# Optimization experiments

Measured on AMD Instinct MI355X. Metric: run time of the kernel, lower is better.

## Reference

```python
import jax, jax.numpy as jnp
import numpy as np

E = 6        # num_experts
C = 256      # embed_dim (expert in_channels)
HID = 256    # mlp_dim (expert hidden_channels)
META = 9
GATE_H = 128
BN_EPS = 1e-5  # torch BatchNorm2d default


def _conv(x, w):
    # x: [1,Cin,H,W], w: [Cout,Cin,3,3] -> [1,Cout,H,W], padding=1
    return jax.lax.conv_general_dilated(
        x, w, window_strides=(1, 1), padding=((1, 1), (1, 1)),
        dimension_numbers=("NCHW", "OIHW", "NCHW"))


def _bn(x, mean, var, gamma, beta):
    # inference-mode BatchNorm2d over channel dim
    scale = gamma * jax.lax.rsqrt(var + BN_EPS)
    return (x - mean[None, :, None, None]) * scale[None, :, None, None] + beta[None, :, None, None]


def setup_inputs() -> dict:
    key = jax.random.key(0)
    ks = jax.random.split(key, 20)
    B, H, W = 16, 64, 64
    f32 = jnp.float32
    return {
        "moe_c4": jax.random.normal(ks[0], (B, C, H, W), f32),
        "meta": jax.random.normal(ks[1], (B, META), f32),
        # Gate MLP: Linear(9,128) -> ReLU -> Linear(128,6)
        "gate_w1": jax.random.normal(ks[2], (META, GATE_H), f32) * 0.3,
        "gate_b1": jnp.zeros((GATE_H,), f32),
        "gate_w2": jax.random.normal(ks[3], (GATE_H, E), f32) * 0.1,
        "gate_b2": jnp.zeros((E,), f32),
        # Expert conv1: Conv2d(C, HID, 3) + BN(HID), stacked over experts
        "conv1_w": jax.random.normal(ks[4], (E, HID, C, 3, 3), f32) * 0.02,
        "conv1_b": jnp.zeros((E, HID), f32),
        "bn1_g": jnp.ones((E, HID), f32) + 0.1 * jax.random.normal(ks[5], (E, HID), f32),
        "bn1_b": 0.1 * jax.random.normal(ks[6], (E, HID), f32),
        "bn1_m": 0.1 * jax.random.normal(ks[7], (E, HID), f32),
        "bn1_v": jax.random.uniform(ks[8], (E, HID), f32) + 0.5,
        # Expert conv2: Conv2d(HID, C, 3) + BN(C)
        "conv2_w": jax.random.normal(ks[9], (E, C, HID, 3, 3), f32) * 0.02,
        "conv2_b": jnp.zeros((E, C), f32),
        "bn2_g": jnp.ones((E, C), f32) + 0.1 * jax.random.normal(ks[10], (E, C), f32),
        "bn2_b": 0.1 * jax.random.normal(ks[11], (E, C), f32),
        "bn2_m": 0.1 * jax.random.normal(ks[12], (E, C), f32),
        "bn2_v": jax.random.uniform(ks[13], (E, C), f32) + 0.5,
    }


def reference(moe_c4, meta, gate_w1, gate_b1, gate_w2, gate_b2,
              conv1_w, conv1_b, bn1_g, bn1_b, bn1_m, bn1_v,
              conv2_w, conv2_b, bn2_g, bn2_b, bn2_m, bn2_v):
    # --- Gate: MLP -> softmax -> top-1 routing ---
    h = jax.nn.relu(meta @ gate_w1 + gate_b1)
    gate_probs = jax.nn.softmax(h @ gate_w2 + gate_b2, axis=-1)  # [B,E]
    top1 = jnp.argmax(gate_probs, axis=-1)                        # [B]

    # --- Dispatch: gather each sample's expert params, run one conv stack per sample ---
    def one(x, w1, b1, g1, be1, m1, v1, w2, b2, g2, be2, m2, v2):
        y = _conv(x[None], w1) + b1[None, :, None, None]
        y = jax.nn.relu(_bn(y, m1, v1, g1, be1))
        y = _conv(y, w2) + b2[None, :, None, None]
        y = jax.nn.relu(_bn(y, m2, v2, g2, be2))
        return y[0]

    out = jax.vmap(one)(
        moe_c4,
        conv1_w[top1], conv1_b[top1], bn1_g[top1], bn1_b[top1], bn1_m[top1], bn1_v[top1],
        conv2_w[top1], conv2_b[top1], bn2_g[top1], bn2_b[top1], bn2_m[top1], bn2_v[top1])

    # --- Load-balance loss (torch.std is unbiased -> ddof=1) ---
    importance = gate_probs.sum(axis=0) / (gate_probs.sum() + 1e-8)
    balance_loss = jnp.std(importance, ddof=1)
    return out, balance_loss
```

## Files before the change

kernel.cpp:

```cpp
#include <hip/hip_runtime.h>
#include <hip/hip_bf16.h>

typedef unsigned short u16;
typedef unsigned int u32;
typedef __attribute__((ext_vector_type(8))) short short8_v;
typedef __attribute__((ext_vector_type(4))) float float4_v;

__device__ __forceinline__ u16 f2bf(float f) {
  u32 u = __float_as_uint(f);
  return (u16)((u + 0x7fffu + ((u >> 16) & 1u)) >> 16);
}

__device__ __forceinline__ void gl_lds16(const void* g, void* l) {
  __builtin_amdgcn_global_load_lds(
      (const __attribute__((address_space(1))) u32*)g,
      (__attribute__((address_space(3))) u32*)l, 16, 0, 0);
}

__global__ void gate_kernel(const float* __restrict__ meta,
                            const float* __restrict__ gw1, const float* __restrict__ gb1,
                            const float* __restrict__ gw2, const float* __restrict__ gb2,
                            int* __restrict__ top1, float* __restrict__ loss_out) {
  const int tid = threadIdx.x;
  __shared__ float logits[16][6];
  __shared__ float red[2][6];
  __shared__ float probs[16][6];
  float w2c[6];
  #pragma unroll
  for (int k = 0; k < 6; ++k) w2c[k] = gw2[tid * 6 + k];
  const float b1v = gb1[tid];
  for (int b = 0; b < 16; ++b) {
    float h = b1v;
    #pragma unroll
    for (int i = 0; i < 9; ++i) h += meta[b * 9 + i] * gw1[i * 128 + tid];
    h = fmaxf(h, 0.f);
    float v[6];
    #pragma unroll
    for (int k = 0; k < 6; ++k) v[k] = h * w2c[k];
    #pragma unroll
    for (int off = 32; off >= 1; off >>= 1)
      #pragma unroll
      for (int k = 0; k < 6; ++k) v[k] += __shfl_down(v[k], off, 64);
    if ((tid & 63) == 0)
      for (int k = 0; k < 6; ++k) red[tid >> 6][k] = v[k];
    __syncthreads();
    if (tid < 6) logits[b][tid] = red[0][tid] + red[1][tid] + gb2[tid];
    __syncthreads();
  }
  if (tid < 16) {
    const int b = tid;
    float m = logits[b][0];
    for (int k = 1; k < 6; ++k) m = fmaxf(m, logits[b][k]);
    float s = 0.f, p[6];
    for (int k = 0; k < 6; ++k) { p[k] = expf(logits[b][k] - m); s += p[k]; }
    int best = 0; float bm = p[0];
    for (int k = 1; k < 6; ++k) if (p[k] > bm) { bm = p[k]; best = k; }
    top1[b] = best;
    for (int k = 0; k < 6; ++k) probs[b][k] = p[k] / s;
  }
  __syncthreads();
  if (tid == 0) {
    float col[6] = {0, 0, 0, 0, 0, 0}, tot = 0.f;
    for (int b = 0; b < 16; ++b)
      for (int k = 0; k < 6; ++k) col[k] += probs[b][k];
    for (int k = 0; k < 6; ++k) tot += col[k];
    float imp[6], mean = 0.f;
    for (int k = 0; k < 6; ++k) { imp[k] = col[k] / (tot + 1e-8f); mean += imp[k]; }
    mean *= (1.f / 6.f);
    float var = 0.f;
    for (int k = 0; k < 6; ++k) { float d = imp[k] - mean; var += d * d; }
    loss_out[0] = sqrtf(var * 0.2f);
  }
}

__global__ void fold_kernel(const float* c1b, const float* g1, const float* be1, const float* m1, const float* v1,
                            const float* c2b, const float* g2, const float* be2, const float* m2, const float* v2,
                            float* fold1, float* fold2) {
  int t = blockIdx.x * 256 + threadIdx.x;
  if (t >= 3072) return;
  int conv = t / 1536, r = t % 1536;
  if (conv == 0) {
    float scale = g1[r] * rsqrtf(v1[r] + 1e-5f);
    float shift = (c1b[r] - m1[r]) * scale + be1[r];
    fold1[r * 2] = scale; fold1[r * 2 + 1] = shift;
  } else {
    float scale = g2[r] * rsqrtf(v2[r] + 1e-5f);
    float shift = (c2b[r] - m2[r]) * scale + be2[r];
    fold2[r * 2] = scale; fold2[r * 2 + 1] = shift;
  }
}

__global__ void wprep_kernel(const float* __restrict__ w1, const float* __restrict__ w2,
                             u16* __restrict__ w1t, u16* __restrict__ w2t) {
  const int tid = threadIdx.x;
  const int conv = blockIdx.x >= 1536 ? 1 : 0;
  const int r = blockIdx.x - (conv ? 1536 : 0);
  const int e = r >> 8, co = r & 255;
  const float* src = (conv ? w2 : w1) + (size_t)r * 2304;
  u16* wdst = conv ? w2t : w1t;
  __shared__ float buf[2304];
  const float4* s4 = (const float4*)src;
  for (int k = tid; k < 576; k += 256) ((float4*)buf)[k] = s4[k];
  __syncthreads();
  for (int j = tid; j < 288; j += 256) {
    int tap = j >> 5, ci0 = (j & 31) * 8;
    u16 v[8];
    #pragma unroll
    for (int i = 0; i < 8; ++i) v[i] = f2bf(buf[(ci0 + i) * 9 + tap]);
    int4 pk;
    pk.x = (int)((u32)v[0] | ((u32)v[1] << 16));
    pk.y = (int)((u32)v[2] | ((u32)v[3] << 16));
    pk.z = (int)((u32)v[4] | ((u32)v[5] << 16));
    pk.w = (int)((u32)v[6] | ((u32)v[7] << 16));
    *(int4*)(wdst + (((size_t)e * 9 + tap) * 256 + co) * 256 + ci0) = pk;
  }
}

__global__ void transpose_pad_kernel(const float* __restrict__ x, u16* __restrict__ xpt) {
  const int b = blockIdx.x >> 6, r = blockIdx.x & 63;
  const int tid = threadIdx.x;
  __shared__ u16 tile[64 * 258];
  const int cg = tid & 15, ci_g = tid >> 4;
  const float4* xb4 = (const float4*)(x + ((size_t)b * 256) * 4096 + r * 64);
  #pragma unroll
  for (int k = 0; k < 16; ++k) {
    int ci = k * 16 + ci_g;
    float4 v = xb4[(size_t)ci * 1024 + cg];
    tile[(cg * 4 + 0) * 258 + ci] = f2bf(v.x);
    tile[(cg * 4 + 1) * 258 + ci] = f2bf(v.y);
    tile[(cg * 4 + 2) * 258 + ci] = f2bf(v.z);
    tile[(cg * 4 + 3) * 258 + ci] = f2bf(v.w);
  }
  __syncthreads();
  u16* dstb = xpt + ((size_t)b * 4356 + (size_t)(r + 1) * 66 + 1) * 256;
  #pragma unroll
  for (int it = 0; it < 8; ++it) {
    int chunk = it * 256 + tid;
    int cc = chunk >> 5, part = chunk & 31;
    const u32* lp = (const u32*)(tile + cc * 258 + part * 8);
    int4 vv = {(int)lp[0], (int)lp[1], (int)lp[2], (int)lp[3]};
    *(int4*)(dstb + (size_t)cc * 256 + part * 8) = vv;
  }
}

__global__ void border_zero_kernel(u16* xpt, u16* hpt) {
  int t = blockIdx.x * 256 + threadIdx.x;
  const int TOT = 2 * 16 * 260 * 32;
  if (t >= TOT) return;
  int buf = t / (16 * 260 * 32);
  int r = t % (16 * 260 * 32);
  int b = r / (260 * 32);
  int r2 = r % (260 * 32);
  int idx = r2 >> 5, part = r2 & 31;
  int rc;
  if (idx < 66) rc = idx;
  else if (idx < 132) rc = 65 * 66 + (idx - 66);
  else { int rem = idx - 132; rc = (1 + (rem >> 1)) * 66 + (rem & 1) * 65; }
  u16* base = buf ? hpt : xpt;
  int4 z = {0, 0, 0, 0};
  *(int4*)(base + ((size_t)b * 4356 + rc) * 256 + part * 8) = z;
}

template <int MODE>
__global__ __launch_bounds__(256, 2) void conv_mfma_kernel(
    const u16* __restrict__ src, const u16* __restrict__ wt,
    const int* __restrict__ top1, const float* __restrict__ fold,
    float* __restrict__ outF, u16* __restrict__ outH) {
  __shared__ char Ab[16384];
  __shared__ char Bb[17408];
  const int tid = threadIdx.x;
  const int lane = tid & 63;
  const int wid = tid >> 6;
  const int wr = wid >> 1, wc = wid & 1;
  const int orig = blockIdx.x;
  const int swz = (orig & 7) * 64 + (orig >> 3);
  const int ptile = swz & 31, b = swz >> 5;
  const int e = top1[b];

  const char* srcB0 = (const char*)src + ((size_t)b * 4356 + (size_t)ptile * 132) * 512;
  const char* wA0 = (const char*)wt + (size_t)e * 9 * 65536 * 2;

  float4_v acc[8][4];
  #pragma unroll
  for (int m = 0; m < 8; ++m)
    #pragma unroll
    for (int n = 0; n < 4; ++n)
      acc[m][n] = (float4_v){0.f, 0.f, 0.f, 0.f};

  for (int chunk = 0; chunk < 8; ++chunk) {
    #pragma unroll
    for (int tap = 0; tap < 9; ++tap) {
      __syncthreads();
      if (tap == 0) {
        const char* sB = srcB0 + chunk * 64;
        const int u0 = wid * 256;
        #pragma unroll
        for (int i = 0; i < 4; ++i) {
          int u = u0 + i * 64 + lane;
          int du = u >> 2;
          int qs = (u & 3) ^ ((u >> 3) & 3);
          gl_lds16(sB + (size_t)du * 512 + qs * 16, Bb + (size_t)(u0 + i * 64) * 16);
        }
        if (wid == 0) {
          int u = 1024 + lane;
          int du = u >> 2;
          int qs = (u & 3) ^ ((u >> 3) & 3);
          gl_lds16(sB + (size_t)du * 512 + qs * 16, Bb + 1024 * 16);
        }
      }
      {
        const char* sA = wA0 + (size_t)tap * 131072 + chunk * 64;
        const int u0 = wid * 256;
        #pragma unroll
        for (int i = 0; i < 4; ++i) {
          int u = u0 + i * 64 + lane;
          int cl = u >> 2;
          int qs = (u & 3) ^ ((u >> 3) & 3);
          gl_lds16(sA + (size_t)cl * 512 + qs * 16, Ab + (size_t)(u0 + i * 64) * 16);
        }
      }
      __syncthreads();

      const int kh = tap / 3, kw = tap % 3;
      short8_v bv[4];
      #pragma unroll
      for (int n = 0; n < 4; ++n) {
        int pt = wc * 64 + n * 16 + (lane & 15);
        int rc = ((pt >> 6) + kh) * 66 + (pt & 63) + kw;
        int slot = (lane >> 4) ^ ((rc >> 1) & 3);
        bv[n] = *(const short8_v*)(Bb + rc * 64 + slot * 16);
      }
      #pragma unroll
      for (int m = 0; m < 8; ++m) {
        int cl = wr * 128 + m * 16 + (lane & 15);
        int slot = (lane >> 4) ^ ((cl >> 1) & 3);
        short8_v avm = *(const short8_v*)(Ab + cl * 64 + slot * 16);
        #pragma unroll
        for (int n = 0; n < 4; ++n)
          acc[m][n] = __builtin_amdgcn_mfma_f32_16x16x32_bf16(avm, bv[n], acc[m][n], 0, 0, 0);
      }
    }
  }

  const float* fe = fold + (size_t)e * 512;
  #pragma unroll
  for (int m = 0; m < 8; ++m) {
    const int cb = wr * 128 + m * 16 + ((lane >> 4) << 2);
    float sc0 = fe[(cb + 0) * 2], sh0 = fe[(cb + 0) * 2 + 1];
    float sc1 = fe[(cb + 1) * 2], sh1 = fe[(cb + 1) * 2 + 1];
    float sc2 = fe[(cb + 2) * 2], sh2 = fe[(cb + 2) * 2 + 1];
    float sc3 = fe[(cb + 3) * 2], sh3 = fe[(cb + 3) * 2 + 1];
    #pragma unroll
    for (int n = 0; n < 4; ++n) {
      const int pt = ptile * 128 + wc * 64 + n * 16 + (lane & 15);
      float v0 = fmaxf(acc[m][n][0] * sc0 + sh0, 0.f);
      float v1 = fmaxf(acc[m][n][1] * sc1 + sh1, 0.f);
      float v2 = fmaxf(acc[m][n][2] * sc2 + sh2, 0.f);
      float v3 = fmaxf(acc[m][n][3] * sc3 + sh3, 0.f);
      if (MODE == 1) {
        const size_t rc = (size_t)((pt >> 6) + 1) * 66 + (pt & 63) + 1;
        uint2 pk;
        pk.x = (u32)f2bf(v0) | ((u32)f2bf(v1) << 16);
        pk.y = (u32)f2bf(v2) | ((u32)f2bf(v3) << 16);
        *(uint2*)(outH + ((size_t)b * 4356 + rc) * 256 + cb) = pk;
      } else {
        float* ob = outF + (size_t)b * 1048576;
        ob[(size_t)(cb + 0) * 4096 + pt] = v0;
        ob[(size_t)(cb + 1) * 4096 + pt] = v1;
        ob[(size_t)(cb + 2) * 4096 + pt] = v2;
        ob[(size_t)(cb + 3) * 4096 + pt] = v3;
      }
    }
  }
}

extern "C" void kernel_launch(void* const* d_in, const int* in_sizes, int n_in,
                              void* d_out, int out_size, void* d_ws, size_t ws_size,
                              hipStream_t stream) {
  const float* x    = (const float*)d_in[0];
  const float* meta = (const float*)d_in[1];
  const float* gw1  = (const float*)d_in[2];
  const float* gb1  = (const float*)d_in[3];
  const float* gw2  = (const float*)d_in[4];
  const float* gb2  = (const float*)d_in[5];
  const float* c1w  = (const float*)d_in[6];
  const float* c1b  = (const float*)d_in[7];
  const float* bn1g = (const float*)d_in[8];
  const float* bn1b = (const float*)d_in[9];
  const float* bn1m = (const float*)d_in[10];
  const float* bn1v = (const float*)d_in[11];
  const float* c2w  = (const float*)d_in[12];
  const float* c2b  = (const float*)d_in[13];
  const float* bn2g = (const float*)d_in[14];
  const float* bn2b = (const float*)d_in[15];
  const float* bn2m = (const float*)d_in[16];
  const float* bn2v = (const float*)d_in[17];

  char* ws = (char*)d_ws;
  u16* xpt   = (u16*)(ws);
  u16* hpt   = (u16*)(ws + 35684352);
  u16* w1t   = (u16*)(ws + 71368704);
  u16* w2t   = (u16*)(ws + 78446592);
  float* fold1 = (float*)(ws + 85524480);
  float* fold2 = (float*)(ws + 85536768);
  int* top1  = (int*)(ws + 85549056);

  float* outF = (float*)d_out;
  float* loss = outF + 16777216;

  hipLaunchKernelGGL(gate_kernel, dim3(1), dim3(128), 0, stream,
                     meta, gw1, gb1, gw2, gb2, top1, loss);
  hipLaunchKernelGGL(fold_kernel, dim3(12), dim3(256), 0, stream,
                     c1b, bn1g, bn1b, bn1m, bn1v, c2b, bn2g, bn2b, bn2m, bn2v, fold1, fold2);
  hipLaunchKernelGGL(wprep_kernel, dim3(3072), dim3(256), 0, stream, c1w, c2w, w1t, w2t);
  hipLaunchKernelGGL(transpose_pad_kernel, dim3(1024), dim3(256), 0, stream, x, xpt);
  hipLaunchKernelGGL(border_zero_kernel, dim3(1040), dim3(256), 0, stream, xpt, hpt);
  hipLaunchKernelGGL((conv_mfma_kernel<1>), dim3(512), dim3(256), 0, stream,
                     xpt, w1t, top1, fold1, (float*)nullptr, hpt);
  hipLaunchKernelGGL((conv_mfma_kernel<2>), dim3(512), dim3(256), 0, stream,
                     hpt, w2t, top1, fold2, outF, (u16*)nullptr);
}
```

Baseline: 339.8 us.

## Double-buffer conv LDS tiles and merge small prep kernels

The conv MFMA kernel now double-buffers both the weight (A) and input (B) LDS tiles, prefetching the next tap/chunk while computing the current one, which removes one barrier per iteration. Two small setup kernels are also merged: gate plus BN-fold run in one block, and transpose plus border-zero run in one launch. Doubling LDS to about 67KB per block may limit occupancy at the requested two blocks per CU. The gate MLP is also parallelised across samples.

After: 347.6 us. 1.02x slower.

```diff
diff --git a/kernel.cpp b/kernel.cpp
--- a/kernel.cpp
+++ b/kernel.cpp
@@ -17,42 +17,79 @@
       (__attribute__((address_space(3))) u32*)l, 16, 0, 0);
 }
 
-__global__ void gate_kernel(const float* __restrict__ meta,
-                            const float* __restrict__ gw1, const float* __restrict__ gb1,
-                            const float* __restrict__ gw2, const float* __restrict__ gb2,
-                            int* __restrict__ top1, float* __restrict__ loss_out) {
+__device__ __forceinline__ void stage_tile_1024(const char* src, char* dst, int wid, int lane) {
+  const int u0 = wid * 256;
+  #pragma unroll
+  for (int i = 0; i < 4; ++i) {
+    int u = u0 + i * 64 + lane;
+    int cl = u >> 2;
+    int qs = (u & 3) ^ ((u >> 3) & 3);
+    gl_lds16(src + (size_t)cl * 512 + qs * 16, dst + (size_t)(u0 + i * 64) * 16);
+  }
+}
+__device__ __forceinline__ void stage_tile_B(const char* src, char* dst, int wid, int lane) {
+  stage_tile_1024(src, dst, wid, lane);
+  if (wid == 0) {
+    int u = 1024 + lane;
+    int du = u >> 2;
+    int qs = (u & 3) ^ ((u >> 3) & 3);
+    gl_lds16(src + (size_t)du * 512 + qs * 16, dst + (size_t)1024 * 16);
+  }
+}
+
+__global__ void gate_fold_kernel(const float* __restrict__ meta,
+                                 const float* __restrict__ gw1, const float* __restrict__ gb1,
+                                 const float* __restrict__ gw2, const float* __restrict__ gb2,
+                                 const float* __restrict__ c1b, const float* __restrict__ g1,
+                                 const float* __restrict__ be1, const float* __restrict__ m1,
+                                 const float* __restrict__ v1,
+                                 const float* __restrict__ c2b, const float* __restrict__ g2,
+                                 const float* __restrict__ be2, const float* __restrict__ m2,
+                                 const float* __restrict__ v2,
+                                 float* __restrict__ fold1, float* __restrict__ fold2,
+                                 int* __restrict__ top1, float* __restrict__ loss_out) {
   const int tid = threadIdx.x;
-  __shared__ float logits[16][6];
-  __shared__ float red[2][6];
   __shared__ float probs[16][6];
-  float w2c[6];
-  #pragma unroll
-  for (int k = 0; k < 6; ++k) w2c[k] = gw2[tid * 6 + k];
-  const float b1v = gb1[tid];
-  for (int b = 0; b < 16; ++b) {
-    float h = b1v;
-    #pragma unroll
-    for (int i = 0; i < 9; ++i) h += meta[b * 9 + i] * gw1[i * 128 + tid];
-    h = fmaxf(h, 0.f);
-    float v[6];
-    #pragma unroll
-    for (int k = 0; k < 6; ++k) v[k] = h * w2c[k];
-    #pragma unroll
-    for (int off = 32; off >= 1; off >>= 1)
-      #pragma unroll
-      for (int k = 0; k < 6; ++k) v[k] += __shfl_down(v[k], off, 64);
-    if ((tid & 63) == 0)
-      for (int k = 0; k < 6; ++k) red[tid >> 6][k] = v[k];
-    __syncthreads();
-    if (tid < 6) logits[b][tid] = red[0][tid] + red[1][tid] + gb2[tid];
-    __syncthreads();
-  }
-  if (tid < 16) {
-    const int b = tid;
-    float m = logits[b][0];
-    for (int k = 1; k < 6; ++k) m = fmaxf(m, logits[b][k]);
+
+  for (int t = tid; t < 3072; t += 1024) {
+    int conv = t >> 11 ? 1 : (t >= 1536 ? 1 : 0);
+    int r = t - (conv ? 1536 : 0);
+    if (conv == 0) {
+      float scale = g1[r] * rsqrtf(v1[r] + 1e-5f);
+      float shift = (c1b[r] - m1[r]) * scale + be1[r];
+      fold1[r * 2] = scale; fold1[r * 2 + 1] = shift;
+    } else {
+      float scale = g2[r] * rsqrtf(v2[r] + 1e-5f);
+      float shift = (c2b[r] - m2[r]) * scale + be2[r];
+      fold2[r * 2] = scale; fold2[r * 2 + 1] = shift;
+    }
+  }
+
+  const int b = tid >> 6, lane = tid & 63;
+  float h0 = gb1[lane], h1 = gb1[lane + 64];
+  #pragma unroll
+  for (int i = 0; i < 9; ++i) {
+    float m = meta[b * 9 + i];
+    h0 += m * gw1[i * 128 + lane];
+    h1 += m * gw1[i * 128 + lane + 64];
+  }
+  h0 = fmaxf(h0, 0.f); h1 = fmaxf(h1, 0.f);
+  float v[6];
+  #pragma unroll
+  for (int k = 0; k < 6; ++k)
+    v[k] = h0 * gw2[lane * 6 + k] + h1 * gw2[(lane + 64) * 6 + k];
+  #pragma unroll
+  for (int off = 32; off >= 1; off >>= 1)
+    #pragma unroll
+    for (int k = 0; k < 6; ++k) v[k] += __shfl_xor(v[k], off, 64);
+  if (lane == 0) {
+    float lg[6];
+    #pragma unroll
+    for (int k = 0; k < 6; ++k) lg[k] = v[k] + gb2[k];
+    float m = lg[0];
+    for (int k = 1; k < 6; ++k) m = fmaxf(m, lg[k]);
     float s = 0.f, p[6];
-    for (int k = 0; k < 6; ++k) { p[k] = expf(logits[b][k] - m); s += p[k]; }
+    for (int k = 0; k < 6; ++k) { p[k] = expf(lg[k] - m); s += p[k]; }
     int best = 0; float bm = p[0];
     for (int k = 1; k < 6; ++k) if (p[k] > bm) { bm = p[k]; best = k; }
     top1[b] = best;
@@ -61,8 +98,8 @@
   __syncthreads();
   if (tid == 0) {
     float col[6] = {0, 0, 0, 0, 0, 0}, tot = 0.f;
-    for (int b = 0; b < 16; ++b)
-      for (int k = 0; k < 6; ++k) col[k] += probs[b][k];
+    for (int bb = 0; bb < 16; ++bb)
+      for (int k = 0; k < 6; ++k) col[k] += probs[bb][k];
     for (int k = 0; k < 6; ++k) tot += col[k];
     float imp[6], mean = 0.f;
     for (int k = 0; k < 6; ++k) { imp[k] = col[k] / (tot + 1e-8f); mean += imp[k]; }
@@ -70,23 +107,6 @@
     float var = 0.f;
     for (int k = 0; k < 6; ++k) { float d = imp[k] - mean; var += d * d; }
     loss_out[0] = sqrtf(var * 0.2f);
-  }
-}
-
-__global__ void fold_kernel(const float* c1b, const float* g1, const float* be1, const float* m1, const float* v1,
-                            const float* c2b, const float* g2, const float* be2, const float* m2, const float* v2,
-                            float* fold1, float* fold2) {
-  int t = blockIdx.x * 256 + threadIdx.x;
-  if (t >= 3072) return;
-  int conv = t / 1536, r = t % 1536;
-  if (conv == 0) {
-    float scale = g1[r] * rsqrtf(v1[r] + 1e-5f);
-    float shift = (c1b[r] - m1[r]) * scale + be1[r];
-    fold1[r * 2] = scale; fold1[r * 2 + 1] = shift;
-  } else {
-    float scale = g2[r] * rsqrtf(v2[r] + 1e-5f);
-    float shift = (c2b[r] - m2[r]) * scale + be2[r];
-    fold2[r * 2] = scale; fold2[r * 2 + 1] = shift;
   }
 }
 
@@ -116,10 +136,27 @@
   }
 }
 
-__global__ void transpose_pad_kernel(const float* __restrict__ x, u16* __restrict__ xpt) {
-  const int b = blockIdx.x >> 6, r = blockIdx.x & 63;
+__global__ void transpose_border_kernel(const float* __restrict__ x, u16* __restrict__ xpt,
+                                        u16* __restrict__ hpt) {
   const int tid = threadIdx.x;
   __shared__ u16 tile[64 * 258];
+  if (blockIdx.x >= 1024) {
+    int t = (blockIdx.x - 1024) * 256 + tid;
+    int buf = t / (16 * 260 * 32);
+    int r = t % (16 * 260 * 32);
+    int b = r / (260 * 32);
+    int r2 = r % (260 * 32);
+    int idx = r2 >> 5, part = r2 & 31;
+    int rc;
+    if (idx < 66) rc = idx;
+    else if (idx < 132) rc = 65 * 66 + (idx - 66);
+    else { int rem = idx - 132; rc = (1 + (rem >> 1)) * 66 + (rem & 1) * 65; }
+    u16* base = buf ? hpt : xpt;
+    int4 z = {0, 0, 0, 0};
+    *(int4*)(base + ((size_t)b * 4356 + rc) * 256 + part * 8) = z;
+    return;
+  }
+  const int b = blockIdx.x >> 6, r = blockIdx.x & 63;
   const int cg = tid & 15, ci_g = tid >> 4;
   const float4* xb4 = (const float4*)(x + ((size_t)b * 256) * 4096 + r * 64);
   #pragma unroll
@@ -143,31 +180,13 @@
   }
 }
 
-__global__ void border_zero_kernel(u16* xpt, u16* hpt) {
-  int t = blockIdx.x * 256 + threadIdx.x;
-  const int TOT = 2 * 16 * 260 * 32;
-  if (t >= TOT) return;
-  int buf = t / (16 * 260 * 32);
-  int r = t % (16 * 260 * 32);
-  int b = r / (260 * 32);
-  int r2 = r % (260 * 32);
-  int idx = r2 >> 5, part = r2 & 31;
-  int rc;
-  if (idx < 66) rc = idx;
-  else if (idx < 132) rc = 65 * 66 + (idx - 66);
-  else { int rem = idx - 132; rc = (1 + (rem >> 1)) * 66 + (rem & 1) * 65; }
-  u16* base = buf ? hpt : xpt;
-  int4 z = {0, 0, 0, 0};
-  *(int4*)(base + ((size_t)b * 4356 + rc) * 256 + part * 8) = z;
-}
-
 template <int MODE>
 __global__ __launch_bounds__(256, 2) void conv_mfma_kernel(
     const u16* __restrict__ src, const u16* __restrict__ wt,
     const int* __restrict__ top1, const float* __restrict__ fold,
     float* __restrict__ outF, u16* __restrict__ outH) {
-  __shared__ char Ab[16384];
-  __shared__ char Bb[17408];
+  __shared__ char Ab[2 * 16384];
+  __shared__ char Bb[2 * 17408];
   const int tid = threadIdx.x;
   const int lane = tid & 63;
   const int wid = tid >> 6;
@@ -187,40 +206,25 @@
     for (int n = 0; n < 4; ++n)
       acc[m][n] = (float4_v){0.f, 0.f, 0.f, 0.f};
 
+  stage_tile_1024(wA0, Ab, wid, lane);
+  stage_tile_B(srcB0, Bb, wid, lane);
+  __syncthreads();
+
   for (int chunk = 0; chunk < 8; ++chunk) {
     #pragma unroll
     for (int tap = 0; tap < 9; ++tap) {
-      __syncthreads();
-      if (tap == 0) {
-        const char* sB = srcB0 + chunk * 64;
-        const int u0 = wid * 256;
-        #pragma unroll
-        for (int i = 0; i < 4; ++i) {
-          int u = u0 + i * 64 + lane;
-          int du = u >> 2;
-          int qs = (u & 3) ^ ((u >> 3) & 3);
-          gl_lds16(sB + (size_t)du * 512 + qs * 16, Bb + (size_t)(u0 + i * 64) * 16);
-        }
-        if (wid == 0) {
-          int u = 1024 + lane;
-          int du = u >> 2;
-          int qs = (u & 3) ^ ((u >> 3) & 3);
-          gl_lds16(sB + (size_t)du * 512 + qs * 16, Bb + 1024 * 16);
-        }
+      const int s_par = (chunk + tap) & 1;
+      if (!(chunk == 7 && tap == 8)) {
+        const int ntap = (tap == 8) ? 0 : tap + 1;
+        const int nchunk = (tap == 8) ? chunk + 1 : chunk;
+        stage_tile_1024(wA0 + (size_t)ntap * 131072 + nchunk * 64,
+                        Ab + (s_par ^ 1) * 16384, wid, lane);
       }
-      {
-        const char* sA = wA0 + (size_t)tap * 131072 + chunk * 64;
-        const int u0 = wid * 256;
-        #pragma unroll
-        for (int i = 0; i < 4; ++i) {
-          int u = u0 + i * 64 + lane;
-          int cl = u >> 2;
-          int qs = (u & 3) ^ ((u >> 3) & 3);
-          gl_lds16(sA + (size_t)cl * 512 + qs * 16, Ab + (size_t)(u0 + i * 64) * 16);
-        }
-      }
-      __syncthreads();
-
+      if (tap == 0 && chunk < 7)
+        stage_tile_B(srcB0 + (chunk + 1) * 64, Bb + ((chunk + 1) & 1) * 17408, wid, lane);
+
+      const char* aB = Ab + s_par * 16384;
+      const char* bB = Bb + (chunk & 1) * 17408;
       const int kh = tap / 3, kw = tap % 3;
       short8_v bv[4];
       #pragma unroll
@@ -228,17 +232,18 @@
         int pt = wc * 64 + n * 16 + (lane & 15);
         int rc = ((pt >> 6) + kh) * 66 + (pt & 63) + kw;
         int slot = (lane >> 4) ^ ((rc >> 1) & 3);
-        bv[n] = *(const short8_v*)(Bb + rc * 64 + slot * 16);
+        bv[n] = *(const short8_v*)(bB + rc * 64 + slot * 16);
       }
       #pragma unroll
       for (int m = 0; m < 8; ++m) {
         int cl = wr * 128 + m * 16 + (lane & 15);
         int slot = (lane >> 4) ^ ((cl >> 1) & 3);
-        short8_v avm = *(const short8_v*)(Ab + cl * 64 + slot * 16);
+        short8_v avm = *(const short8_v*)(aB + cl * 64 + slot * 16);
         #pragma unroll
         for (int n = 0; n < 4; ++n)
           acc[m][n] = __builtin_amdgcn_mfma_f32_16x16x32_bf16(avm, bv[n], acc[m][n], 0, 0, 0);
       }
+      __syncthreads();
     }
   }
 
@@ -308,13 +313,12 @@
   float* outF = (float*)d_out;
   float* loss = outF + 16777216;
 
-  hipLaunchKernelGGL(gate_kernel, dim3(1), dim3(128), 0, stream,
-                     meta, gw1, gb1, gw2, gb2, top1, loss);
-  hipLaunchKernelGGL(fold_kernel, dim3(12), dim3(256), 0, stream,
-                     c1b, bn1g, bn1b, bn1m, bn1v, c2b, bn2g, bn2b, bn2m, bn2v, fold1, fold2);
+  hipLaunchKernelGGL(gate_fold_kernel, dim3(1), dim3(1024), 0, stream,
+                     meta, gw1, gb1, gw2, gb2,
+                     c1b, bn1g, bn1b, bn1m, bn1v, c2b, bn2g, bn2b, bn2m, bn2v,
+                     fold1, fold2, top1, loss);
   hipLaunchKernelGGL(wprep_kernel, dim3(3072), dim3(256), 0, stream, c1w, c2w, w1t, w2t);
-  hipLaunchKernelGGL(transpose_pad_kernel, dim3(1024), dim3(256), 0, stream, x, xpt);
-  hipLaunchKernelGGL(border_zero_kernel, dim3(1040), dim3(256), 0, stream, xpt, hpt);
+  hipLaunchKernelGGL(transpose_border_kernel, dim3(2064), dim3(256), 0, stream, x, xpt, hpt);
   hipLaunchKernelGGL((conv_mfma_kernel<1>), dim3(512), dim3(256), 0, stream,
                      xpt, w1t, top1, fold1, (float*)nullptr, hpt);
   hipLaunchKernelGGL((conv_mfma_kernel<2>), dim3(512), dim3(256), 0, stream,
```
